# Kernel tuning notes

Measured on AMD Instinct MI355X. Metric: run time of the kernel, lower is better.

## Reference

```python
import jax, jax.numpy as jnp
import numpy as np

IN_DIM, HID_DIM, OUT_DIM, N_EXP = 1024, 4096, 1024, 8
BATCH = 8192


def setup_inputs() -> dict:
    key = jax.random.key(0)
    ks = jax.random.split(key, 8)
    s_in = 1.0 / np.sqrt(IN_DIM)
    s_hid = 1.0 / np.sqrt(HID_DIM)
    return {
        "x": jax.random.normal(ks[0], (BATCH, IN_DIM), jnp.float32),
        "router_w": jax.random.uniform(ks[1], (IN_DIM, N_EXP), jnp.float32, -s_in, s_in),
        "router_b": jax.random.uniform(ks[2], (N_EXP,), jnp.float32, -s_in, s_in),
        "expert_w": jax.random.uniform(ks[3], (N_EXP, IN_DIM, HID_DIM), jnp.float32, -s_in, s_in),
        "expert_b": jax.random.uniform(ks[4], (N_EXP, HID_DIM), jnp.float32, -s_in, s_in),
        "proj_w": jax.random.uniform(ks[5], (HID_DIM, OUT_DIM), jnp.float32, -s_hid, s_hid),
        "proj_b": jax.random.uniform(ks[6], (OUT_DIM,), jnp.float32, -s_hid, s_hid),
    }


def reference(x, router_w, router_b, expert_w, expert_b, proj_w, proj_b):
    # Hard routing: argmax over router logits selects one expert per token.
    logits = x @ router_w + router_b                 # [N, E]
    idx = jnp.argmax(logits, axis=-1)                # [N] int
    n_exp = expert_w.shape[0]
    # Masked per-expert GEMMs (loop over small fixed expert count), summed.
    h = jnp.zeros((x.shape[0], expert_w.shape[2]), dtype=x.dtype)
    for e in range(n_exp):
        mask = (idx == e)[:, None]                   # [N, 1]
        h = h + jnp.where(mask, x @ expert_w[e] + expert_b[e], 0.0)
    out = h @ proj_w + proj_b                        # [N, out_dim]
    routing_weights = jax.nn.one_hot(idx, n_exp, dtype=jnp.float32)
    return out, routing_weights
```

## Files before the change

### kernel.cpp

```cpp
#include <hip/hip_runtime.h>
#include <stdint.h>

#define B_TOK 8192
#define DIN 1024
#define DHID 4096
#define DOUT 1024
#define NE 8

typedef __bf16 bf16x8 __attribute__((ext_vector_type(8)));
typedef float f32x4 __attribute__((ext_vector_type(4)));

__device__ __forceinline__ unsigned short f2bf(float f) {
  union { float f; unsigned u; } v; v.f = f;
  unsigned r = v.u + 0x7fffu + ((v.u >> 16) & 1u);
  return (unsigned short)(r >> 16);
}

__device__ __forceinline__ void async16(const void* g, void* l) {
  __builtin_amdgcn_global_load_lds(
      (__attribute__((address_space(1))) void*)const_cast<void*>(g),
      (__attribute__((address_space(3))) void*)l, 16, 0, 0);
}

__global__ __launch_bounds__(256) void router_kernel(
    const float* __restrict__ x, const float* __restrict__ rw,
    const float* __restrict__ rb, float* __restrict__ oh,
    unsigned short* __restrict__ xb, int* __restrict__ idx,
    int* __restrict__ pos, int* __restrict__ counts)
{
  const int token = blockIdx.x * 4 + (threadIdx.x >> 6);
  const int lane = threadIdx.x & 63;
  const float* xrow = x + (size_t)token * DIN;
  double acc[NE];
#pragma unroll
  for (int e = 0; e < NE; ++e) acc[e] = 0.0;

#pragma unroll
  for (int j = 0; j < 4; ++j) {
    const int v4 = j * 64 + lane;
    const float4 xv = ((const float4*)xrow)[v4];
    const float4* rwr = (const float4*)(rw + (size_t)v4 * 32);
#pragma unroll
    for (int c = 0; c < 4; ++c) {
      const float xs = (&xv.x)[c];
      const float4 w0 = rwr[c * 2 + 0];
      const float4 w1 = rwr[c * 2 + 1];
      acc[0] += (double)(xs * w0.x); acc[1] += (double)(xs * w0.y);
      acc[2] += (double)(xs * w0.z); acc[3] += (double)(xs * w0.w);
      acc[4] += (double)(xs * w1.x); acc[5] += (double)(xs * w1.y);
      acc[6] += (double)(xs * w1.z); acc[7] += (double)(xs * w1.w);
    }
    ushort4 us;
    us.x = f2bf(xv.x); us.y = f2bf(xv.y); us.z = f2bf(xv.z); us.w = f2bf(xv.w);
    ((ushort4*)(xb + (size_t)token * DIN))[v4] = us;
  }
#pragma unroll
  for (int off = 32; off > 0; off >>= 1)
#pragma unroll
    for (int e = 0; e < NE; ++e) acc[e] += __shfl_xor(acc[e], off, 64);

  if (lane == 0) {
    double best = -1e300; int be = 0;
#pragma unroll
    for (int e = 0; e < NE; ++e) {
      const double v = acc[e] + (double)rb[e];
      if (v > best) { best = v; be = e; }
    }
    idx[token] = be;
    pos[token] = atomicAdd(&counts[be], 1);
    float* o = oh + (size_t)token * NE;
#pragma unroll
    for (int e = 0; e < NE; ++e) o[e] = (e == be) ? 1.f : 0.f;
  }
}

__global__ __launch_bounds__(256) void transpose_bf16(
    const float* __restrict__ in, unsigned short* __restrict__ out, int K, int N)
{
  __shared__ float tile[64][65];
  const size_t mat = (size_t)blockIdx.z * (size_t)K * N;
  const int k0 = blockIdx.x * 64, n0 = blockIdx.y * 64;
  const int c = threadIdx.x & 63, r0 = threadIdx.x >> 6;
#pragma unroll
  for (int rr = 0; rr < 64; rr += 4)
    tile[rr + r0][c] = in[mat + (size_t)(k0 + rr + r0) * N + n0 + c];
  __syncthreads();
#pragma unroll
  for (int rr = 0; rr < 64; rr += 4) {
    const int n2 = rr + r0;
    out[mat + (size_t)(n0 + n2) * K + k0 + c] = f2bf(tile[c][n2]);
  }
}

__global__ void slots_kernel(const int* __restrict__ counts, int* __restrict__ offsets,
                             int* __restrict__ slot_e, int* __restrict__ slot_g0,
                             int* __restrict__ slot_nr, int* __restrict__ nslots)
{
  int off = 0, s = 0;
  offsets[0] = 0;
  for (int e = 0; e < NE; ++e) {
    const int c = counts[e];
    for (int t = 0; t < c; t += 128) {
      slot_e[s] = e; slot_g0[s] = off + t;
      slot_nr[s] = (c - t < 128) ? (c - t) : 128;
      ++s;
    }
    off += c;
    offsets[e + 1] = off;
  }
  *nslots = s;
}

__global__ __launch_bounds__(256) void scatter_kernel(
    const int* __restrict__ idx, const int* __restrict__ pos,
    const int* __restrict__ offsets, int* __restrict__ perm)
{
  const int t = blockIdx.x * 256 + threadIdx.x;
  perm[offsets[idx[t]] + pos[t]] = t;
}

__global__ __launch_bounds__(256) void expert_gemm(
    const unsigned short* __restrict__ xb, const unsigned short* __restrict__ Wt,
    const float* __restrict__ eb, const int* __restrict__ perm,
    const int* __restrict__ slot_e, const int* __restrict__ slot_g0,
    const int* __restrict__ slot_nr, const int* __restrict__ nslots,
    unsigned short* __restrict__ h)
{
  const int id = blockIdx.x;
  const int s = id >> 5;
  const int ntile = id & 31;
  if (s >= *nslots) return;
  const int e = slot_e[s];
  const int g0 = slot_g0[s];
  const int nr = slot_nr[s];
  const int n0 = ntile * 128;

  __shared__ __align__(16) unsigned short lsA[128 * 64];
  __shared__ __align__(16) unsigned short lsB[128 * 64];

  const int tid = threadIdx.x;
  const int w = tid >> 6, lane = tid & 63;
  const int rgrp = lane >> 3, cch = lane & 7;
  const int sw8 = (cch ^ rgrp) * 8;
  const int rowb = w * 32;

  int tok[4];
#pragma unroll
  for (int sub = 0; sub < 4; ++sub) {
    const int row = rowb + sub * 8 + rgrp;
    tok[sub] = (row < nr) ? perm[g0 + row] : -1;
  }
  const unsigned short* wb = Wt + (size_t)e * DHID * DIN;

  const f32x4 z = {0.f, 0.f, 0.f, 0.f};
  f32x4 acc[4][4];
#pragma unroll
  for (int i = 0; i < 4; ++i)
#pragma unroll
    for (int j = 0; j < 4; ++j) acc[i][j] = z;

  const int wm = (w & 1) * 64, wn = (w >> 1) * 64;
  const int quad = lane >> 4, l15 = lane & 15;
  int ma[4], nb[4];
#pragma unroll
  for (int i = 0; i < 4; ++i) { ma[i] = wm + i * 16 + l15; nb[i] = wn + i * 16 + l15; }

  for (int k0 = 0; k0 < DIN; k0 += 64) {
#pragma unroll
    for (int sub = 0; sub < 4; ++sub) {
      const int rbase = rowb + sub * 8;
      if (tok[sub] >= 0)
        async16(xb + (size_t)tok[sub] * DIN + k0 + sw8, &lsA[rbase * 64]);
      async16(wb + (size_t)(n0 + rbase + rgrp) * DIN + k0 + sw8, &lsB[rbase * 64]);
    }
    __syncthreads();
#pragma unroll
    for (int ks = 0; ks < 2; ++ks) {
      const int q = ks * 4 + quad;
      bf16x8 af[4], bfr[4];
#pragma unroll
      for (int i = 0; i < 4; ++i)
        af[i] = *(const bf16x8*)&lsA[ma[i] * 64 + ((q ^ (ma[i] & 7)) << 3)];
#pragma unroll
      for (int i = 0; i < 4; ++i)
        bfr[i] = *(const bf16x8*)&lsB[nb[i] * 64 + ((q ^ (nb[i] & 7)) << 3)];
#pragma unroll
      for (int i = 0; i < 4; ++i)
#pragma unroll
        for (int j = 0; j < 4; ++j)
          acc[i][j] = __builtin_amdgcn_mfma_f32_16x16x32_bf16(af[i], bfr[j], acc[i][j], 0, 0, 0);
    }
    __syncthreads();
  }

#pragma unroll
  for (int j = 0; j < 4; ++j) {
    const int col = n0 + nb[j];
    const float bias = eb[e * DHID + col];
#pragma unroll
    for (int i = 0; i < 4; ++i)
#pragma unroll
      for (int r2 = 0; r2 < 4; ++r2) {
        const int row = wm + i * 16 + quad * 4 + r2;
        if (row < nr)
          h[(size_t)(g0 + row) * DHID + col] = f2bf(acc[i][j][r2] + bias);
      }
  }
}

__global__ __launch_bounds__(256) void proj_gemm(
    const unsigned short* __restrict__ hm, const unsigned short* __restrict__ Pt,
    const float* __restrict__ pb, const int* __restrict__ perm,
    float* __restrict__ out)
{
  const int id = blockIdx.x;
  const int m0 = (id & 63) * 128;
  const int n0 = (id >> 6) * 128;
  __shared__ __align__(16) unsigned short lsA[128 * 64];
  __shared__ __align__(16) unsigned short lsB[128 * 64];

  const int tid = threadIdx.x;
  const int w = tid >> 6, lane = tid & 63;
  const int rgrp = lane >> 3, cch = lane & 7;
  const int sw8 = (cch ^ rgrp) * 8;
  const int rowb = w * 32;

  const f32x4 z = {0.f, 0.f, 0.f, 0.f};
  f32x4 acc[4][4];
#pragma unroll
  for (int i = 0; i < 4; ++i)
#pragma unroll
    for (int j = 0; j < 4; ++j) acc[i][j] = z;

  const int wm = (w & 1) * 64, wn = (w >> 1) * 64;
  const int quad = lane >> 4, l15 = lane & 15;
  int ma[4], nb[4];
#pragma unroll
  for (int i = 0; i < 4; ++i) { ma[i] = wm + i * 16 + l15; nb[i] = wn + i * 16 + l15; }

  for (int k0 = 0; k0 < DHID; k0 += 64) {
#pragma unroll
    for (int sub = 0; sub < 4; ++sub) {
      const int rbase = rowb + sub * 8;
      async16(hm + (size_t)(m0 + rbase + rgrp) * DHID + k0 + sw8, &lsA[rbase * 64]);
      async16(Pt + (size_t)(n0 + rbase + rgrp) * DHID + k0 + sw8, &lsB[rbase * 64]);
    }
    __syncthreads();
#pragma unroll
    for (int ks = 0; ks < 2; ++ks) {
      const int q = ks * 4 + quad;
      bf16x8 af[4], bfr[4];
#pragma unroll
      for (int i = 0; i < 4; ++i)
        af[i] = *(const bf16x8*)&lsA[ma[i] * 64 + ((q ^ (ma[i] & 7)) << 3)];
#pragma unroll
      for (int i = 0; i < 4; ++i)
        bfr[i] = *(const bf16x8*)&lsB[nb[i] * 64 + ((q ^ (nb[i] & 7)) << 3)];
#pragma unroll
      for (int i = 0; i < 4; ++i)
#pragma unroll
        for (int j = 0; j < 4; ++j)
          acc[i][j] = __builtin_amdgcn_mfma_f32_16x16x32_bf16(af[i], bfr[j], acc[i][j], 0, 0, 0);
    }
    __syncthreads();
  }

#pragma unroll
  for (int i = 0; i < 4; ++i)
#pragma unroll
    for (int r2 = 0; r2 < 4; ++r2) {
      const int row = m0 + wm + i * 16 + quad * 4 + r2;
      const int orow = perm[row];
#pragma unroll
      for (int j = 0; j < 4; ++j) {
        const int col = n0 + nb[j];
        out[(size_t)orow * DOUT + col] = acc[i][j][r2] + pb[col];
      }
    }
}

extern "C" void kernel_launch(void* const* d_in, const int* in_sizes, int n_in,
                              void* d_out, int out_size, void* d_ws, size_t ws_size,
                              hipStream_t stream)
{
  const float* x  = (const float*)d_in[0];
  const float* rw = (const float*)d_in[1];
  const float* rb = (const float*)d_in[2];
  const float* ew = (const float*)d_in[3];
  const float* eb = (const float*)d_in[4];
  const float* pw = (const float*)d_in[5];
  const float* pb = (const float*)d_in[6];
  float* out = (float*)d_out;
  float* oh  = out + (size_t)B_TOK * DOUT;

  char* ws = (char*)d_ws;
  constexpr size_t OXB = 0;
  constexpr size_t OWT = OXB + (size_t)B_TOK * DIN * 2;
  constexpr size_t OPT = OWT + (size_t)NE * DHID * DIN * 2;
  constexpr size_t OH  = OPT + (size_t)DOUT * DHID * 2;
  constexpr size_t OIDX = OH + (size_t)B_TOK * DHID * 2;
  constexpr size_t OPOS = OIDX + (size_t)B_TOK * 4;
  constexpr size_t OPRM = OPOS + (size_t)B_TOK * 4;
  constexpr size_t OCNT = OPRM + (size_t)B_TOK * 4;
  constexpr size_t OOFF = OCNT + 256;
  constexpr size_t OSE  = OOFF + 256;
  constexpr size_t OSG  = OSE + 512;
  constexpr size_t OSN  = OSG + 512;
  constexpr size_t ONS  = OSN + 512;
  constexpr size_t NEED = ONS + 512;

  if (ws_size < NEED) {
    hipMemsetAsync(d_out, 0, (size_t)out_size * 4, stream);
    return;
  }

  unsigned short* xb   = (unsigned short*)(ws + OXB);
  unsigned short* Wt   = (unsigned short*)(ws + OWT);
  unsigned short* Pt   = (unsigned short*)(ws + OPT);
  unsigned short* h    = (unsigned short*)(ws + OH);
  int* idx     = (int*)(ws + OIDX);
  int* pos     = (int*)(ws + OPOS);
  int* perm    = (int*)(ws + OPRM);
  int* counts  = (int*)(ws + OCNT);
  int* offsets = (int*)(ws + OOFF);
  int* slot_e  = (int*)(ws + OSE);
  int* slot_g0 = (int*)(ws + OSG);
  int* slot_nr = (int*)(ws + OSN);
  int* nslots  = (int*)(ws + ONS);

  hipMemsetAsync(counts, 0, 64, stream);
  router_kernel<<<B_TOK / 4, 256, 0, stream>>>(x, rw, rb, oh, xb, idx, pos, counts);
  transpose_bf16<<<dim3(DIN / 64, DHID / 64, NE), 256, 0, stream>>>(ew, Wt, DIN, DHID);
  transpose_bf16<<<dim3(DHID / 64, DOUT / 64, 1), 256, 0, stream>>>(pw, Pt, DHID, DOUT);
  slots_kernel<<<1, 1, 0, stream>>>(counts, offsets, slot_e, slot_g0, slot_nr, nslots);
  scatter_kernel<<<B_TOK / 256, 256, 0, stream>>>(idx, pos, offsets, perm);
  expert_gemm<<<72 * 32, 256, 0, stream>>>(
      xb, Wt, eb, perm, slot_e, slot_g0, slot_nr, nslots, h);
  proj_gemm<<<(B_TOK / 128) * (DOUT / 128), 256, 0, stream>>>(h, Pt, pb, perm, out);
}
```

Measured before the change: 574.7 us.

## Double-buffer LDS tiles in expert and projection GEMMs to overlap loads with MFMA

Both GEMM kernels now use two LDS buffers per operand. The next K-tile's async global-to-LDS loads are issued before computing on the current tile, with an explicit vmcnt wait so only the current tile's loads must complete. This hides global memory latency behind MFMA work. It doubles LDS use to 64KB per block, which may reduce occupancy. Padding rows in the expert GEMM now load a valid token row instead of being skipped, which makes the per-thread load count uniform for the vmcnt accounting.

```diff
diff --git a/kernel.cpp b/kernel.cpp
--- a/kernel.cpp
+++ b/kernel.cpp
@@ -135,8 +135,8 @@
   const int nr = slot_nr[s];
   const int n0 = ntile * 128;
 
-  __shared__ __align__(16) unsigned short lsA[128 * 64];
-  __shared__ __align__(16) unsigned short lsB[128 * 64];
+  __shared__ __align__(16) unsigned short lsA[2][128 * 64];
+  __shared__ __align__(16) unsigned short lsB[2][128 * 64];
 
   const int tid = threadIdx.x;
   const int w = tid >> 6, lane = tid & 63;
@@ -148,7 +148,7 @@
 #pragma unroll
   for (int sub = 0; sub < 4; ++sub) {
     const int row = rowb + sub * 8 + rgrp;
-    tok[sub] = (row < nr) ? perm[g0 + row] : -1;
+    tok[sub] = perm[g0 + (row < nr ? row : 0)];
   }
   const unsigned short* wb = Wt + (size_t)e * DHID * DIN;
 
@@ -165,32 +165,50 @@
 #pragma unroll
   for (int i = 0; i < 4; ++i) { ma[i] = wm + i * 16 + l15; nb[i] = wn + i * 16 + l15; }
 
-  for (int k0 = 0; k0 < DIN; k0 += 64) {
+  auto stage = [&](int bsel, int k0) {
 #pragma unroll
     for (int sub = 0; sub < 4; ++sub) {
       const int rbase = rowb + sub * 8;
-      if (tok[sub] >= 0)
-        async16(xb + (size_t)tok[sub] * DIN + k0 + sw8, &lsA[rbase * 64]);
-      async16(wb + (size_t)(n0 + rbase + rgrp) * DIN + k0 + sw8, &lsB[rbase * 64]);
-    }
-    __syncthreads();
+      async16(xb + (size_t)tok[sub] * DIN + k0 + sw8, &lsA[bsel][rbase * 64]);
+      async16(wb + (size_t)(n0 + rbase + rgrp) * DIN + k0 + sw8, &lsB[bsel][rbase * 64]);
+    }
+  };
+
+  stage(0, 0);
+  constexpr int NT = DIN / 64;
+  for (int kt = 0; kt < NT; ++kt) {
+    const int cur = kt & 1;
+    if (kt + 1 < NT) {
+      stage(cur ^ 1, (kt + 1) * 64);
+      __builtin_amdgcn_sched_barrier(0);
+      asm volatile("s_waitcnt vmcnt(8)" ::: "memory");
+    } else {
+      __builtin_amdgcn_sched_barrier(0);
+      asm volatile("s_waitcnt vmcnt(0)" ::: "memory");
+    }
+    __builtin_amdgcn_sched_barrier(0);
+    __builtin_amdgcn_s_barrier();
+    __builtin_amdgcn_sched_barrier(0);
+
 #pragma unroll
     for (int ks = 0; ks < 2; ++ks) {
       const int q = ks * 4 + quad;
       bf16x8 af[4], bfr[4];
 #pragma unroll
       for (int i = 0; i < 4; ++i)
-        af[i] = *(const bf16x8*)&lsA[ma[i] * 64 + ((q ^ (ma[i] & 7)) << 3)];
-#pragma unroll
-      for (int i = 0; i < 4; ++i)
-        bfr[i] = *(const bf16x8*)&lsB[nb[i] * 64 + ((q ^ (nb[i] & 7)) << 3)];
+        af[i] = *(const bf16x8*)&lsA[cur][ma[i] * 64 + ((q ^ (ma[i] & 7)) << 3)];
+#pragma unroll
+      for (int i = 0; i < 4; ++i)
+        bfr[i] = *(const bf16x8*)&lsB[cur][nb[i] * 64 + ((q ^ (nb[i] & 7)) << 3)];
 #pragma unroll
       for (int i = 0; i < 4; ++i)
 #pragma unroll
         for (int j = 0; j < 4; ++j)
           acc[i][j] = __builtin_amdgcn_mfma_f32_16x16x32_bf16(af[i], bfr[j], acc[i][j], 0, 0, 0);
     }
-    __syncthreads();
+    __builtin_amdgcn_sched_barrier(0);
+    __builtin_amdgcn_s_barrier();
+    __builtin_amdgcn_sched_barrier(0);
   }
 
 #pragma unroll
@@ -216,8 +234,8 @@
   const int id = blockIdx.x;
   const int m0 = (id & 63) * 128;
   const int n0 = (id >> 6) * 128;
-  __shared__ __align__(16) unsigned short lsA[128 * 64];
-  __shared__ __align__(16) unsigned short lsB[128 * 64];
+  __shared__ __align__(16) unsigned short lsA[2][128 * 64];
+  __shared__ __align__(16) unsigned short lsB[2][128 * 64];
 
   const int tid = threadIdx.x;
   const int w = tid >> 6, lane = tid & 63;
@@ -238,31 +256,50 @@
 #pragma unroll
   for (int i = 0; i < 4; ++i) { ma[i] = wm + i * 16 + l15; nb[i] = wn + i * 16 + l15; }
 
-  for (int k0 = 0; k0 < DHID; k0 += 64) {
+  auto stage = [&](int bsel, int k0) {
 #pragma unroll
     for (int sub = 0; sub < 4; ++sub) {
       const int rbase = rowb + sub * 8;
-      async16(hm + (size_t)(m0 + rbase + rgrp) * DHID + k0 + sw8, &lsA[rbase * 64]);
-      async16(Pt + (size_t)(n0 + rbase + rgrp) * DHID + k0 + sw8, &lsB[rbase * 64]);
-    }
-    __syncthreads();
+      async16(hm + (size_t)(m0 + rbase + rgrp) * DHID + k0 + sw8, &lsA[bsel][rbase * 64]);
+      async16(Pt + (size_t)(n0 + rbase + rgrp) * DHID + k0 + sw8, &lsB[bsel][rbase * 64]);
+    }
+  };
+
+  stage(0, 0);
+  constexpr int NT = DHID / 64;
+  for (int kt = 0; kt < NT; ++kt) {
+    const int cur = kt & 1;
+    if (kt + 1 < NT) {
+      stage(cur ^ 1, (kt + 1) * 64);
+      __builtin_amdgcn_sched_barrier(0);
+      asm volatile("s_waitcnt vmcnt(8)" ::: "memory");
+    } else {
+      __builtin_amdgcn_sched_barrier(0);
+      asm volatile("s_waitcnt vmcnt(0)" ::: "memory");
+    }
+    __builtin_amdgcn_sched_barrier(0);
+    __builtin_amdgcn_s_barrier();
+    __builtin_amdgcn_sched_barrier(0);
+
 #pragma unroll
     for (int ks = 0; ks < 2; ++ks) {
       const int q = ks * 4 + quad;
       bf16x8 af[4], bfr[4];
 #pragma unroll
       for (int i = 0; i < 4; ++i)
-        af[i] = *(const bf16x8*)&lsA[ma[i] * 64 + ((q ^ (ma[i] & 7)) << 3)];
-#pragma unroll
-      for (int i = 0; i < 4; ++i)
-        bfr[i] = *(const bf16x8*)&lsB[nb[i] * 64 + ((q ^ (nb[i] & 7)) << 3)];
+        af[i] = *(const bf16x8*)&lsA[cur][ma[i] * 64 + ((q ^ (ma[i] & 7)) << 3)];
+#pragma unroll
+      for (int i = 0; i < 4; ++i)
+        bfr[i] = *(const bf16x8*)&lsB[cur][nb[i] * 64 + ((q ^ (nb[i] & 7)) << 3)];
 #pragma unroll
       for (int i = 0; i < 4; ++i)
 #pragma unroll
         for (int j = 0; j < 4; ++j)
           acc[i][j] = __builtin_amdgcn_mfma_f32_16x16x32_bf16(af[i], bfr[j], acc[i][j], 0, 0, 0);
     }
-    __syncthreads();
+    __builtin_amdgcn_sched_barrier(0);
+    __builtin_amdgcn_s_barrier();
+    __builtin_amdgcn_sched_barrier(0);
   }
 
 #pragma unroll
```

Result: slower. 588.5 us (+2.4%).
